# Kernel tuning notes

Hardware: AMD Instinct MI355X
Metric: run time of the kernel (lower is better)

Reference implementation:

```python
import jax, jax.numpy as jnp
import numpy as np

UNITS = 1024
INPUT_DIM = 2048
OUTPUT_DIM = 1000
EPS = 0.01
DT = 0.1
BATCH = 8192


def _kaiming_like(key, shape, fan_in):
    # matches torch kaiming_uniform_(a=sqrt(5)) bound = sqrt(6/((1+5)*fan_in)) = 1/sqrt(fan_in)
    bound = 1.0 / np.sqrt(fan_in)
    return jax.random.uniform(key, shape, jnp.float32, -bound, bound)


def setup_inputs() -> dict:
    key = jax.random.key(0)
    ks = jax.random.split(key, 12)
    x = jax.random.normal(ks[0], (BATCH, INPUT_DIM), jnp.float32)
    W_in = _kaiming_like(ks[1], (UNITS, INPUT_DIM), INPUT_DIM)
    b_in = _kaiming_like(ks[2], (UNITS,), INPUT_DIM)
    W1 = _kaiming_like(ks[3], (UNITS, UNITS), UNITS)
    b1 = _kaiming_like(ks[4], (UNITS,), UNITS)
    W2 = _kaiming_like(ks[5], (UNITS, UNITS), UNITS)
    b2 = _kaiming_like(ks[6], (UNITS,), UNITS)
    W3 = _kaiming_like(ks[7], (UNITS, UNITS), UNITS)
    b3 = _kaiming_like(ks[8], (UNITS,), UNITS)
    W_out = _kaiming_like(ks[9], (OUTPUT_DIM, UNITS), UNITS)
    b_out = _kaiming_like(ks[10], (OUTPUT_DIM,), UNITS)
    return {"x": x, "W_in": W_in, "b_in": b_in, "W1": W1, "b1": b1,
            "W2": W2, "b2": b2, "W3": W3, "b3": b3,
            "W_out": W_out, "b_out": b_out}


def transnet_layer(z, W, b):
    # z: (B, 2U). Implicit layer: A y = rhs, output = C y - rhs (== -y mathematically)
    U = W.shape[0]
    u_in, v_in = z[:, :U], z[:, U:]
    relu_u = jax.nn.relu(u_in)
    rhs_u = u_in + DT * b                      # (B, U)
    rhs_v = v_in + (DT / EPS) * relu_u         # (B, U)
    rhs = jnp.concatenate([rhs_u, rhs_v], axis=1)  # (B, 2U)
    eye = jnp.eye(U, dtype=z.dtype)
    A = jnp.block([[eye, DT * W],
                   [-DT * W.T, (1.0 + DT / EPS) * eye]])  # (2U, 2U), batch-independent
    # factor once, solve against all batch rhs columns at once
    y = jnp.linalg.solve(A, rhs.T).T           # (B, 2U)
    u, v = y[:, :U], y[:, U:]
    u_out = DT * (v @ W.T) - u_in - DT * b
    v_out = -DT * (u @ W) + (DT / EPS) * v - v_in - (DT / EPS) * relu_u
    return jnp.concatenate([u_out, v_out], axis=1)


def reference(x, W_in, b_in, W1, b1, W2, b2, W3, b3, W_out, b_out):
    z = x @ W_in.T + b_in                      # (B, U)
    z = jnp.concatenate([z, jax.nn.relu(z)], axis=1)  # (B, 2U)
    z = transnet_layer(z, W1, b1)
    z = transnet_layer(z, W2, b2)
    z = transnet_layer(z, W3, b3)
    z = z[:, :UNITS]
    logits = jax.nn.softmax(z @ W_out.T + b_out, axis=1)
    return logits
```

## Files before the change

### kernel.cpp

```cpp
#include <hip/hip_runtime.h>
#include <hip/hip_bf16.h>
#include <cstdint>


typedef __bf16 bf16;
typedef __bf16 bf16x4 __attribute__((ext_vector_type(4)));
typedef __bf16 bf16x8 __attribute__((ext_vector_type(8)));
typedef float  f32x4  __attribute__((ext_vector_type(4)));

#define C_DT    0.1f
#define C_DTEPS 10.0f
#define C_DINV  (1.0f/11.0f)
#define C_MSC   (0.01f/121.0f)

__device__ __forceinline__ void async_load16(const bf16* g, bf16* l) {
    __builtin_amdgcn_global_load_lds(
        (__attribute__((address_space(1))) void*)(g),
        (__attribute__((address_space(3))) void*)(l),
        16, 0, 0);
}

__device__ __forceinline__ void remap_block(int& bx, int& by) {
    if (gridDim.y == 64) {
        const int lin  = by * 8 + bx;
        const int xcd  = lin & 7;
        const int slot = lin >> 3;
        by = xcd * 8 + (slot & 7);
        bx = slot >> 3;
    }
}

template<int EPI>
__global__ __launch_bounds__(256, 2)
void gemm_bt(const bf16* __restrict__ A, const bf16* __restrict__ B,
             float* __restrict__ out_f,
             bf16* __restrict__ out_b1, bf16* __restrict__ out_b2,
             const float* __restrict__ e0, const float* __restrict__ e1,
             const float* __restrict__ e2,
             int M, int N, int K, int lda, int ldb,
             int ldf, int ld1, int ld2, float sgn,
             long zsA, long zsB, long zs1, long zs2)
{
    __shared__ __attribute__((aligned(16))) char smem[32768];
    bf16* sAe = (bf16*)smem;
    bf16* sBe = (bf16*)(smem + 16384);

    const int t    = threadIdx.x;
    const int wave = t >> 6;
    const int lane = t & 63;
    int bx = blockIdx.x, by = blockIdx.y;
    remap_block(bx, by);
    const long zb = blockIdx.z;
    A += zb * zsA;
    B += zb * zsB;
    if (out_b1) out_b1 += zb * zs1;
    if (out_b2) out_b2 += zb * zs2;

    const long row0 = (long)by * 128;
    const long col0 = (long)bx * 128;
    const int wr = wave >> 1, wc = wave & 1;

    f32x4 acc[4][4];
#pragma unroll
    for (int i = 0; i < 4; i++)
#pragma unroll
        for (int j = 0; j < 4; j++)
            acc[i][j] = f32x4{0.f, 0.f, 0.f, 0.f};

    const int  q  = t >> 2;
    const int  gp = ((t & 3) + 4 - ((q + (q >> 2)) & 3)) & 3;
    const bf16* gA = A + (row0 + q) * (long)lda + gp * 8;
    const bf16* gB = B + (col0 + q) * (long)ldb + gp * 8;

    const int l15  = lane & 15;
    const int fch  = ((lane >> 4) + l15 + (l15 >> 2)) & 3;
    const int aoff = (wr * 64 + l15) * 32 + fch * 8;
    const int boff = (wc * 64 + l15) * 32 + fch * 8;

    auto stage = [&](int buf, int k0) {
        bf16* dA = sAe + buf * 4096 + wave * 512;
        bf16* dB = sBe + buf * 4096 + wave * 512;
        async_load16(gA + k0,                     dA);
        async_load16(gA + 64 * (long)lda + k0,    dA + 2048);
        async_load16(gB + k0,                     dB);
        async_load16(gB + 64 * (long)ldb + k0,    dB + 2048);
    };

    const int nIter = K >> 5;
    stage(0, 0);
    __syncthreads();
    for (int k = 0; k < nIter; k++) {
        const int cur = k & 1;
        if (k + 1 < nIter) stage(cur ^ 1, (k + 1) << 5);

        bf16x8 af[4], bfv[4];
#pragma unroll
        for (int i = 0; i < 4; i++)
            af[i] = *(const bf16x8*)(sAe + cur * 4096 + aoff + i * 16 * 32);
#pragma unroll
        for (int j = 0; j < 4; j++)
            bfv[j] = *(const bf16x8*)(sBe + cur * 4096 + boff + j * 16 * 32);
#pragma unroll
        for (int i = 0; i < 4; i++)
#pragma unroll
            for (int j = 0; j < 4; j++)
                acc[i][j] = __builtin_amdgcn_mfma_f32_16x16x32_bf16(
                    af[i], bfv[j], acc[i][j], 0, 0, 0);

        __syncthreads();
    }

    float* epi = (float*)smem + wave * 1024;
    const int wbase = (lane >> 4) * 256 + (l15 >> 2) * 4 + (l15 & 3);

#pragma unroll
    for (int i = 0; i < 4; i++) {
#pragma unroll
        for (int j = 0; j < 4; j++)
#pragma unroll
            for (int r = 0; r < 4; r++)
                epi[wbase + r * 64 + 16 * j] = acc[i][j][r];

#pragma unroll
        for (int qq = 0; qq < 4; qq++) {
            const f32x4 a4 = ((const f32x4*)epi)[qq * 64 + lane];
            const long m = row0 + wr * 64 + i * 16 + qq * 4 + (lane >> 4);
            const long n = col0 + wc * 64 + 4 * l15;

            if (EPI == 0) {
                const f32x4 b1 = *(const f32x4*)(e1 + n);
                const f32x4 b2 = *(const f32x4*)(e2 + n);
                f32x4 tv; bf16x4 rv, hv;
#pragma unroll
                for (int e = 0; e < 4; e++) {
                    tv[e] = a4[e] + b1[e];
                    rv[e] = (bf16)(11.f * fmaxf(tv[e], 0.f));
                    hv[e] = (bf16)(tv[e] + C_DT * b2[e]);
                }
                *(f32x4*)(out_f + m * (long)ldf + n)    = tv;
                *(bf16x4*)(out_b1 + m * (long)ld1 + n)  = rv;
                *(bf16x4*)(out_b2 + m * (long)ld2 + n)  = hv;
            } else if (EPI == 1) {
                bf16x4 ov;
#pragma unroll
                for (int e = 0; e < 4; e++)
                    ov[e] = (bf16)(((m == n + e) ? C_DINV : 0.f) - C_MSC * a4[e]);
                *(bf16x4*)(out_b1 + m * (long)ld1 + n) = ov;
                *(bf16x4*)(out_b2 + m * (long)ld2 + n) = ov;
            } else if (EPI == 2) {
                bf16x4 ov, o2;
#pragma unroll
                for (int e = 0; e < 4; e++) {
                    ov[e] = (bf16)(sgn * a4[e]);
                    o2[e] = (bf16)(C_DT * sgn * a4[e]);
                }
                *(bf16x4*)(out_b1 + m * (long)ld1 + n) = ov;
                if (out_b2) *(bf16x4*)(out_b2 + m * (long)ld2 + n) = o2;
            } else {
                const f32x4 u0 = *(const f32x4*)(e0 + m * (long)ldf + n);
                const f32x4 b1 = *(const f32x4*)(e1 + n);
                bf16x4 hv, lv;
#pragma unroll
                for (int e = 0; e < 4; e++) {
                    float un = sgn * a4[e] - u0[e] - C_DT * b1[e];
                    bf16 h = (bf16)un;
                    hv[e] = h;
                    lv[e] = (bf16)(un - (float)h);
                }
                *(bf16x4*)(out_b1 + m * (long)ld1 + n) = hv;
                *(bf16x4*)(out_b2 + m * (long)ld2 + n) = lv;
            }
        }
    }
}

__global__ __launch_bounds__(256, 2)
void gemm_layer(const bf16* __restrict__ A, const bf16* __restrict__ B1,
                const bf16* __restrict__ B2, float* __restrict__ u,
                bf16* __restrict__ ACo,
                const float* __restrict__ bl, const float* __restrict__ bn)
{
    __shared__ __attribute__((aligned(16))) char smem[49152];
    bf16* sA  = (bf16*)smem;
    bf16* sB1 = (bf16*)(smem + 16384);
    bf16* sB2 = (bf16*)(smem + 32768);

    const int t    = threadIdx.x;
    const int wave = t >> 6;
    const int lane = t & 63;
    int bx = blockIdx.x, by = blockIdx.y;
    remap_block(bx, by);
    const long row0 = (long)by * 128;
    const long col0 = (long)bx * 128;
    const int wr = wave >> 1, wc = wave & 1;

    f32x4 accU[4][4], accV[4][4];
#pragma unroll
    for (int i = 0; i < 4; i++)
#pragma unroll
        for (int j = 0; j < 4; j++) {
            accU[i][j] = f32x4{0.f, 0.f, 0.f, 0.f};
            accV[i][j] = f32x4{0.f, 0.f, 0.f, 0.f};
        }

    const int  q  = t >> 2;
    const int  gp = ((t & 3) + 4 - ((q + (q >> 2)) & 3)) & 3;
    const bf16* gA  = A  + (row0 + q) * 2048 + gp * 8;
    const bf16* gB1 = B1 + (col0 + q) * 2048 + gp * 8;
    const bf16* gB2 = B2 + (col0 + q) * 2048 + gp * 8;

    const int l15  = lane & 15;
    const int fch  = ((lane >> 4) + l15 + (l15 >> 2)) & 3;
    const int aoff = (wr * 64 + l15) * 32 + fch * 8;
    const int boff = (wc * 64 + l15) * 32 + fch * 8;

    auto stage = [&](int buf, int k0) {
        bf16* dA  = sA  + buf * 4096 + wave * 512;
        bf16* dB1 = sB1 + buf * 4096 + wave * 512;
        bf16* dB2 = sB2 + buf * 4096 + wave * 512;
        async_load16(gA  + k0,             dA);
        async_load16(gA  + 64 * 2048 + k0, dA + 2048);
        async_load16(gB1 + k0,             dB1);
        async_load16(gB1 + 64 * 2048 + k0, dB1 + 2048);
        async_load16(gB2 + k0,             dB2);
        async_load16(gB2 + 64 * 2048 + k0, dB2 + 2048);
    };

    stage(0, 0);
    __syncthreads();
    for (int k = 0; k < 64; k++) {
        const int cur = k & 1;
        if (k + 1 < 64) stage(cur ^ 1, (k + 1) << 5);

        bf16x8 af[4], b1v[4], b2v[4];
#pragma unroll
        for (int i = 0; i < 4; i++)
            af[i] = *(const bf16x8*)(sA + cur * 4096 + aoff + i * 16 * 32);
#pragma unroll
        for (int j = 0; j < 4; j++) {
            b1v[j] = *(const bf16x8*)(sB1 + cur * 4096 + boff + j * 16 * 32);
            b2v[j] = *(const bf16x8*)(sB2 + cur * 4096 + boff + j * 16 * 32);
        }
#pragma unroll
        for (int i = 0; i < 4; i++)
#pragma unroll
            for (int j = 0; j < 4; j++) {
                accV[i][j] = __builtin_amdgcn_mfma_f32_16x16x32_bf16(
                    af[i], b1v[j], accV[i][j], 0, 0, 0);
                accU[i][j] = __builtin_amdgcn_mfma_f32_16x16x32_bf16(
                    af[i], b2v[j], accU[i][j], 0, 0, 0);
            }
        __syncthreads();
    }

    float* epi = (float*)smem + wave * 1024;
    const int wbase = (lane >> 4) * 256 + (l15 >> 2) * 4 + (l15 & 3);

#pragma unroll
    for (int i = 0; i < 4; i++) {
#pragma unroll
        for (int j = 0; j < 4; j++)
#pragma unroll
            for (int r = 0; r < 4; r++)
                epi[wbase + r * 64 + 16 * j] = accV[i][j][r];
        f32x4 v4[4];
#pragma unroll
        for (int qq = 0; qq < 4; qq++)
            v4[qq] = ((const f32x4*)epi)[qq * 64 + lane];
#pragma unroll
        for (int j = 0; j < 4; j++)
#pragma unroll
            for (int r = 0; r < 4; r++)
                epi[wbase + r * 64 + 16 * j] = accU[i][j][r];

#pragma unroll
        for (int qq = 0; qq < 4; qq++) {
            const f32x4 a4 = ((const f32x4*)epi)[qq * 64 + lane];
            const long m  = row0 + wr * 64 + i * 16 + qq * 4 + (lane >> 4);
            const long n  = col0 + wc * 64 + 4 * l15;
            const long iu = m * 1024 + n;
            const f32x4 u0 = *(const f32x4*)(u + iu);
            const f32x4 c1 = *(const f32x4*)(bl + n);
            const f32x4 c2 = *(const f32x4*)(bn + n);
            f32x4 un; bf16x4 rv, hv;
#pragma unroll
            for (int e = 0; e < 4; e++) {
                un[e] = a4[e] - u0[e] - C_DT * c1[e];
                rv[e] = (bf16)(C_DTEPS * fmaxf(un[e], 0.f) - v4[qq][e]);
                hv[e] = (bf16)(un[e] + C_DT * c2[e]);
            }
            *(f32x4*)(u + iu) = un;
            *(bf16x4*)(ACo + m * 2048 + n)        = rv;
            *(bf16x4*)(ACo + m * 2048 + 1024 + n) = hv;
        }
    }
}

__global__ __launch_bounds__(256, 2)
void gemm_split(const bf16* __restrict__ Ah, const bf16* __restrict__ Al,
                const bf16* __restrict__ Bh, const bf16* __restrict__ Bl,
                float* __restrict__ out, const float* __restrict__ bias,
                int M, int N, int K, int blim)
{
    __shared__ __attribute__((aligned(16))) char smem[65536];
    bf16* sAh = (bf16*)smem;
    bf16* sAl = (bf16*)(smem + 16384);
    bf16* sBh = (bf16*)(smem + 32768);
    bf16* sBl = (bf16*)(smem + 49152);

    const int t    = threadIdx.x;
    const int wave = t >> 6;
    const int lane = t & 63;
    int bx = blockIdx.x, by = blockIdx.y;
    remap_block(bx, by);
    const long row0 = (long)by * 128;
    const long col0 = (long)bx * 128;
    const int wr = wave >> 1, wc = wave & 1;

    f32x4 acc[4][4];
#pragma unroll
    for (int i = 0; i < 4; i++)
#pragma unroll
        for (int j = 0; j < 4; j++)
            acc[i][j] = f32x4{0.f, 0.f, 0.f, 0.f};

    const int  q  = t >> 2;
    const int  gp = ((t & 3) + 4 - ((q + (q >> 2)) & 3)) & 3;
    const long gao = (row0 + q) * (long)K + gp * 8;
    const long gbo = (col0 + q) * (long)K + gp * 8;

    const int l15  = lane & 15;
    const int fch  = ((lane >> 4) + l15 + (l15 >> 2)) & 3;
    const int aoff = (wr * 64 + l15) * 32 + fch * 8;
    const int boff = (wc * 64 + l15) * 32 + fch * 8;

    auto stage = [&](int buf, int k0) {
        const int d = buf * 4096 + wave * 512;
        async_load16(Ah + gao + k0,                 sAh + d);
        async_load16(Ah + gao + 64 * (long)K + k0,  sAh + d + 2048);
        async_load16(Al + gao + k0,                 sAl + d);
        async_load16(Al + gao + 64 * (long)K + k0,  sAl + d + 2048);
        async_load16(Bh + gbo + k0,                 sBh + d);
        async_load16(Bh + gbo + 64 * (long)K + k0,  sBh + d + 2048);
        async_load16(Bl + gbo + k0,                 sBl + d);
        async_load16(Bl + gbo + 64 * (long)K + k0,  sBl + d + 2048);
    };

    const int nIter = K >> 5;
    stage(0, 0);
    __syncthreads();
    for (int k = 0; k < nIter; k++) {
        const int cur = k & 1;
        if (k + 1 < nIter) stage(cur ^ 1, (k + 1) << 5);

        bf16x8 ah[4], al[4], bh[4], bl[4];
#pragma unroll
        for (int i = 0; i < 4; i++) {
            ah[i] = *(const bf16x8*)(sAh + cur * 4096 + aoff + i * 16 * 32);
            al[i] = *(const bf16x8*)(sAl + cur * 4096 + aoff + i * 16 * 32);
        }
#pragma unroll
        for (int j = 0; j < 4; j++) {
            bh[j] = *(const bf16x8*)(sBh + cur * 4096 + boff + j * 16 * 32);
            bl[j] = *(const bf16x8*)(sBl + cur * 4096 + boff + j * 16 * 32);
        }
#pragma unroll
        for (int i = 0; i < 4; i++)
#pragma unroll
            for (int j = 0; j < 4; j++) {
                acc[i][j] = __builtin_amdgcn_mfma_f32_16x16x32_bf16(
                    ah[i], bh[j], acc[i][j], 0, 0, 0);
                acc[i][j] = __builtin_amdgcn_mfma_f32_16x16x32_bf16(
                    ah[i], bl[j], acc[i][j], 0, 0, 0);
                acc[i][j] = __builtin_amdgcn_mfma_f32_16x16x32_bf16(
                    al[i], bh[j], acc[i][j], 0, 0, 0);
            }
        __syncthreads();
    }

    float* epi = (float*)smem + wave * 1024;
    const int wbase = (lane >> 4) * 256 + (l15 >> 2) * 4 + (l15 & 3);

#pragma unroll
    for (int i = 0; i < 4; i++) {
#pragma unroll
        for (int j = 0; j < 4; j++)
#pragma unroll
            for (int r = 0; r < 4; r++)
                epi[wbase + r * 64 + 16 * j] = acc[i][j][r];

#pragma unroll
        for (int qq = 0; qq < 4; qq++) {
            f32x4 a4 = ((const f32x4*)epi)[qq * 64 + lane];
            const long m = row0 + wr * 64 + i * 16 + qq * 4 + (lane >> 4);
            const long n = col0 + wc * 64 + 4 * l15;
            f32x4 bv = f32x4{0.f, 0.f, 0.f, 0.f};
            if (n < blim) bv = *(const f32x4*)(bias + n);
#pragma unroll
            for (int e = 0; e < 4; e++) a4[e] += bv[e];
            *(f32x4*)(out + m * (long)N + n) = a4;
        }
    }
}

__global__ void conv_xw(const float* __restrict__ x, bf16* __restrict__ xb,
                        const float* __restrict__ w, bf16* __restrict__ wb)
{
    const long bid = blockIdx.x;
    const float* in;
    bf16* outp;
    long i4;
    if (bid < 16384) { in = x; outp = xb; i4 = bid * 256 + threadIdx.x; }
    else             { in = w; outp = wb; i4 = (bid - 16384) * 256 + threadIdx.x; }
    const f32x4 v = ((const f32x4*)in)[i4];
    bf16x4 o;
#pragma unroll
    for (int e = 0; e < 4; e++) o[e] = (bf16)v[e];
    ((bf16x4*)outp)[i4] = o;
}

__global__ void prep_w3(const float* __restrict__ w0, const float* __restrict__ w1,
                        const float* __restrict__ w2, bf16* __restrict__ Wb,
                        bf16* __restrict__ Wtb)
{
    __shared__ float tile[32][33];
    const int z = blockIdx.z;
    const float* W = (z == 0) ? w0 : (z == 1) ? w1 : w2;
    const long zo = (long)z * 1024 * 1024;
    const int bx = blockIdx.x * 32, by = blockIdx.y * 32;
    const int tx = threadIdx.x & 31, ty = threadIdx.x >> 5;
#pragma unroll
    for (int i = 0; i < 32; i += 8) {
        float v = W[(long)(by + ty + i) * 1024 + bx + tx];
        tile[ty + i][tx] = v;
        Wb[zo + (long)(by + ty + i) * 1024 + bx + tx] = (bf16)v;
    }
    __syncthreads();
#pragma unroll
    for (int i = 0; i < 32; i += 8)
        Wtb[zo + (long)(bx + ty + i) * 1024 + by + tx] = (bf16)tile[tx][ty + i];
}

__global__ void prep_wout(const float* __restrict__ w, bf16* __restrict__ wh,
                          bf16* __restrict__ wl)
{
    const long i4   = (long)blockIdx.x * 256 + threadIdx.x;
    const long base = i4 * 4;
    const int  nrow = (int)(base >> 10);
    bf16x4 h, l;
    if (nrow < 1000) {
        const f32x4 v = ((const f32x4*)w)[i4];
#pragma unroll
        for (int e = 0; e < 4; e++) {
            bf16 hh = (bf16)v[e];
            h[e] = hh;
            l[e] = (bf16)(v[e] - (float)hh);
        }
    } else {
#pragma unroll
        for (int e = 0; e < 4; e++) { h[e] = (bf16)0.f; l[e] = (bf16)0.f; }
    }
    ((bf16x4*)wh)[i4] = h;
    ((bf16x4*)wl)[i4] = l;
}

__global__ __launch_bounds__(256)
void softmax_rows(const float* __restrict__ logits, float* __restrict__ out)
{
    const int row = blockIdx.x;
    const float* lp = logits + (long)row * 1024;
    const int t = threadIdx.x;
    float v[4];
    float mx = -1e30f;
#pragma unroll
    for (int i = 0; i < 4; i++) {
        const int c = t + i * 256;
        v[i] = (c < 1000) ? lp[c] : -1e30f;
        mx = fmaxf(mx, v[i]);
    }
#pragma unroll
    for (int off = 32; off; off >>= 1)
        mx = fmaxf(mx, __shfl_xor(mx, off));
    __shared__ float sm[4], ss[4];
    const int wave = t >> 6;
    if ((t & 63) == 0) sm[wave] = mx;
    __syncthreads();
    mx = fmaxf(fmaxf(sm[0], sm[1]), fmaxf(sm[2], sm[3]));
    float sum = 0.f;
#pragma unroll
    for (int i = 0; i < 4; i++) {
        v[i] = __expf(v[i] - mx);
        sum += v[i];
    }
#pragma unroll
    for (int off = 32; off; off >>= 1)
        sum += __shfl_xor(sum, off);
    if ((t & 63) == 0) ss[wave] = sum;
    __syncthreads();
    const float inv = 1.f / (ss[0] + ss[1] + ss[2] + ss[3]);
#pragma unroll
    for (int i = 0; i < 4; i++) {
        const int c = t + i * 256;
        if (c < 1000) out[(long)row * 1000 + c] = v[i] * inv;
    }
}

extern "C" void kernel_launch(void* const* d_in, const int* in_sizes, int n_in,
                              void* d_out, int out_size, void* d_ws, size_t ws_size,
                              hipStream_t stream)
{
    const float* x     = (const float*)d_in[0];
    const float* W_in  = (const float*)d_in[1];
    const float* b_in  = (const float*)d_in[2];
    const float* Ws[3] = {(const float*)d_in[3], (const float*)d_in[5], (const float*)d_in[7]};
    const float* bs[3] = {(const float*)d_in[4], (const float*)d_in[6], (const float*)d_in[8]};
    const float* W_out = (const float*)d_in[9];
    const float* b_out = (const float*)d_in[10];
    float* out = (float*)d_out;

    char* ws = (char*)d_ws;
    const size_t MB = 1u << 20;
    const long M1 = 1024L * 1024;
    bf16*  xb    = (bf16*)(ws);
    bf16*  Wtbf  = (bf16*)(ws);
    bf16*  Minv  = (bf16*)(ws +  6 * MB);
    bf16*  Pmat  = (bf16*)(ws + 12 * MB);
    bf16*  Bcat  = (bf16*)(ws + 18 * MB);
    bf16*  zh    = (bf16*)(ws);
    bf16*  zl    = (bf16*)(ws + 16 * MB);
    bf16*  Winb  = (bf16*)(ws + 32 * MB);
    bf16*  Wouth = (bf16*)(ws + 36 * MB);
    bf16*  Woutl = (bf16*)(ws + 38 * MB);
    bf16*  Wbf   = (bf16*)(ws + 40 * MB);
    bf16*  Ccat  = (bf16*)(ws + 46 * MB);
    float* u     = (float*)(ws + 58 * MB);
    float* logits= (float*)(ws + 58 * MB);
    bf16*  AC_a  = (bf16*)(ws + 90 * MB);
    bf16*  AC_b  = (bf16*)(ws + 122 * MB);

    const dim3 blk(256);
    const dim3 gBig(8, 64);
    const dim3 gSm3(8, 8, 3);
    const dim3 gT3(32, 32, 3);

    conv_xw<<<18432, blk, 0, stream>>>(x, xb, W_in, Winb);
    prep_wout<<<1024, blk, 0, stream>>>(W_out, Wouth, Woutl);

    gemm_bt<0><<<gBig, blk, 0, stream>>>(xb, Winb, u, AC_a, AC_a + 1024,
                                         nullptr, b_in, bs[0],
                                         8192, 1024, 2048, 2048, 2048,
                                         1024, 2048, 2048, 1.f, 0, 0, 0, 0);

    prep_w3<<<gT3, blk, 0, stream>>>(Ws[0], Ws[1], Ws[2], Wbf, Wtbf);
    gemm_bt<1><<<gSm3, blk, 0, stream>>>(Wtbf, Wtbf, nullptr, Minv, Bcat,
                                         nullptr, nullptr, nullptr,
                                         1024, 1024, 1024, 1024, 1024,
                                         0, 1024, 2048, 1.f, M1, M1, M1, 2 * M1);
    gemm_bt<2><<<gSm3, blk, 0, stream>>>(Minv, Wbf, nullptr, Bcat + 1024, nullptr,
                                         nullptr, nullptr, nullptr,
                                         1024, 1024, 1024, 1024, 1024,
                                         0, 2048, 0, C_DT, M1, M1, 2 * M1, 0);
    gemm_bt<2><<<gSm3, blk, 0, stream>>>(Wbf, Minv, nullptr, Pmat, Ccat,
                                         nullptr, nullptr, nullptr,
                                         1024, 1024, 1024, 1024, 1024,
                                         0, 1024, 2048, 1.f, M1, M1, M1, 2 * M1);
    gemm_bt<2><<<gSm3, blk, 0, stream>>>(Pmat, Wbf, nullptr, Ccat + 1024, nullptr,
                                         nullptr, nullptr, nullptr,
                                         1024, 1024, 1024, 1024, 1024,
                                         0, 2048, 0, 0.01f, M1, M1, 2 * M1, 0);

    gemm_layer<<<gBig, blk, 0, stream>>>(AC_a, Bcat, Ccat, u, AC_b, bs[0], bs[1]);
    gemm_layer<<<gBig, blk, 0, stream>>>(AC_b, Bcat + 2 * M1, Ccat + 2 * M1,
                                         u, AC_a, bs[1], bs[2]);
    gemm_bt<5><<<gBig, blk, 0, stream>>>(AC_a, Ccat + 4 * M1, nullptr, zh, zl,
                                         u, bs[2], nullptr,
                                         8192, 1024, 2048, 2048, 2048,
                                         1024, 1024, 1024, 1.f, 0, 0, 0, 0);

    gemm_split<<<gBig, blk, 0, stream>>>(zh, zl, Wouth, Woutl, logits, b_out,
                                         8192, 1024, 1024, 1000);
    softmax_rows<<<8192, blk, 0, stream>>>(logits, out);
}
```

Measured before the change: 534.2 us.

## Rewrite layer GEMM with 8-wave 256x128 tiles and interleaved async prefetch

Replaces the 4-wave 128x128 layer GEMM with an 8-wave kernel that computes a 256x128 tile and uses a K-step of 64 with an XOR-swizzled LDS layout. Prefetch of the next stage is split into four chunks, each issued between the MFMA phases, with explicit vmcnt/lgkmcnt waits, barriers and s_setprio raised around the MFMA blocks. The aim is better reuse of B per A load, fewer global loads, and tighter overlap of memory traffic with matrix math. In exchange it uses 128KB of LDS per block, which limits occupancy, and it drops the block remapping.

```diff
diff --git a/kernel.cpp b/kernel.cpp
--- a/kernel.cpp
+++ b/kernel.cpp
@@ -174,117 +174,200 @@
     }
 }
 
-__global__ __launch_bounds__(256, 2)
-void gemm_layer(const bf16* __restrict__ A, const bf16* __restrict__ B1,
-                const bf16* __restrict__ B2, float* __restrict__ u,
-                bf16* __restrict__ ACo,
-                const float* __restrict__ bl, const float* __restrict__ bn)
-{
-    __shared__ __attribute__((aligned(16))) char smem[49152];
-    bf16* sA  = (bf16*)smem;
-    bf16* sB1 = (bf16*)(smem + 16384);
-    bf16* sB2 = (bf16*)(smem + 32768);
+__global__ __launch_bounds__(512, 2)
+void gemm_layer8(const bf16* __restrict__ A, const bf16* __restrict__ B1,
+                 const bf16* __restrict__ B2, float* __restrict__ u,
+                 bf16* __restrict__ ACo,
+                 const float* __restrict__ bl, const float* __restrict__ bn)
+{
+    __shared__ __attribute__((aligned(16))) bf16 sm[65536];
 
     const int t    = threadIdx.x;
     const int wave = t >> 6;
     const int lane = t & 63;
-    int bx = blockIdx.x, by = blockIdx.y;
-    remap_block(bx, by);
-    const long row0 = (long)by * 128;
+    const int l15  = lane & 15;
+    const int lq   = lane >> 4;
+    const int bx = blockIdx.x;
+    const int by = blockIdx.y;
+    const long row0 = (long)by * 256;
     const long col0 = (long)bx * 128;
-    const int wr = wave >> 1, wc = wave & 1;
-
-    f32x4 accU[4][4], accV[4][4];
-#pragma unroll
-    for (int i = 0; i < 4; i++)
-#pragma unroll
-        for (int j = 0; j < 4; j++) {
+    const int wr = wave >> 2;
+    const int wc = wave & 3;
+
+    f32x4 accV[8][2], accU[8][2];
+#pragma unroll
+    for (int i = 0; i < 8; i++)
+#pragma unroll
+        for (int j = 0; j < 2; j++) {
+            accV[i][j] = f32x4{0.f, 0.f, 0.f, 0.f};
             accU[i][j] = f32x4{0.f, 0.f, 0.f, 0.f};
-            accV[i][j] = f32x4{0.f, 0.f, 0.f, 0.f};
-        }
-
-    const int  q  = t >> 2;
-    const int  gp = ((t & 3) + 4 - ((q + (q >> 2)) & 3)) & 3;
-    const bf16* gA  = A  + (row0 + q) * 2048 + gp * 8;
-    const bf16* gB1 = B1 + (col0 + q) * 2048 + gp * 8;
-    const bf16* gB2 = B2 + (col0 + q) * 2048 + gp * 8;
-
-    const int l15  = lane & 15;
-    const int fch  = ((lane >> 4) + l15 + (l15 >> 2)) & 3;
-    const int aoff = (wr * 64 + l15) * 32 + fch * 8;
-    const int boff = (wc * 64 + l15) * 32 + fch * 8;
-
-    auto stage = [&](int buf, int k0) {
-        bf16* dA  = sA  + buf * 4096 + wave * 512;
-        bf16* dB1 = sB1 + buf * 4096 + wave * 512;
-        bf16* dB2 = sB2 + buf * 4096 + wave * 512;
-        async_load16(gA  + k0,             dA);
-        async_load16(gA  + 64 * 2048 + k0, dA + 2048);
-        async_load16(gB1 + k0,             dB1);
-        async_load16(gB1 + 64 * 2048 + k0, dB1 + 2048);
-        async_load16(gB2 + k0,             dB2);
-        async_load16(gB2 + 64 * 2048 + k0, dB2 + 2048);
+        }
+
+    const int tr = t >> 3;
+    const int sg = (t & 7) ^ (tr & 7);
+    const bf16* gA  = A  + (row0 + tr) * 2048 + sg * 8;
+    const bf16* gB1 = B1 + (col0 + tr) * 2048 + sg * 8;
+    const bf16* gB2 = B2 + (col0 + tr) * 2048 + sg * 8;
+    bf16* const ldA  = sm + wave * 512;
+    bf16* const ldB1 = sm + 32768 + wave * 512;
+    bf16* const ldB2 = sm + 49152 + wave * 512;
+
+    auto stA = [&](int buf, int ci, int k0) {
+        async_load16(gA + (long)ci * 131072 + k0, ldA + buf * 16384 + ci * 4096);
     };
-
-    stage(0, 0);
-    __syncthreads();
-    for (int k = 0; k < 64; k++) {
-        const int cur = k & 1;
-        if (k + 1 < 64) stage(cur ^ 1, (k + 1) << 5);
-
-        bf16x8 af[4], b1v[4], b2v[4];
-#pragma unroll
-        for (int i = 0; i < 4; i++)
-            af[i] = *(const bf16x8*)(sA + cur * 4096 + aoff + i * 16 * 32);
-#pragma unroll
-        for (int j = 0; j < 4; j++) {
-            b1v[j] = *(const bf16x8*)(sB1 + cur * 4096 + boff + j * 16 * 32);
-            b2v[j] = *(const bf16x8*)(sB2 + cur * 4096 + boff + j * 16 * 32);
-        }
-#pragma unroll
-        for (int i = 0; i < 4; i++)
-#pragma unroll
-            for (int j = 0; j < 4; j++) {
-                accV[i][j] = __builtin_amdgcn_mfma_f32_16x16x32_bf16(
-                    af[i], b1v[j], accV[i][j], 0, 0, 0);
-                accU[i][j] = __builtin_amdgcn_mfma_f32_16x16x32_bf16(
-                    af[i], b2v[j], accU[i][j], 0, 0, 0);
+    auto stB1v = [&](int buf, int cb, int k0) {
+        async_load16(gB1 + (long)cb * 131072 + k0, ldB1 + buf * 8192 + cb * 4096);
+    };
+    auto stB2v = [&](int buf, int cb, int k0) {
+        async_load16(gB2 + (long)cb * 131072 + k0, ldB2 + buf * 8192 + cb * 4096);
+    };
+
+    const int sl0 = lq ^ (l15 & 7);
+    const int sl1 = (4 + lq) ^ (l15 & 7);
+    const int aro = l15 * 64;
+    const int cbo = (wc >> 1) * 4096;
+    const int bro = ((wc & 1) * 32 + l15) * 64;
+
+    stA(0, 0, 0); stA(0, 2, 0);
+    stB1v(0, 0, 0); stB1v(0, 1, 0);
+    stB2v(0, 0, 0); stB2v(0, 1, 0);
+    stA(0, 1, 0); stA(0, 3, 0);
+
+    for (int kt = 0; kt < 32; ++kt) {
+        const int  cur = kt & 1, nb = cur ^ 1;
+        const bool st  = kt < 31;
+        const int  k0n = (kt + 1) << 6;
+        const bf16* bA  = sm + cur * 16384;
+        const bf16* bB1 = sm + 32768 + cur * 8192;
+        const bf16* bB2 = sm + 49152 + cur * 8192;
+        bf16x8 a[4], b1k[2], b2k[2];
+
+        if (st) asm volatile("s_waitcnt vmcnt(2)" ::: "memory");
+        else    asm volatile("s_waitcnt vmcnt(0)" ::: "memory");
+        __builtin_amdgcn_s_barrier();
+#pragma unroll
+        for (int fi = 0; fi < 4; ++fi)
+            a[fi] = *(const bf16x8*)(bA + wr * 8192 + fi * 1024 + aro + sl0 * 8);
+#pragma unroll
+        for (int fj = 0; fj < 2; ++fj) {
+            b1k[fj] = *(const bf16x8*)(bB1 + cbo + fj * 1024 + bro + sl0 * 8);
+            b2k[fj] = *(const bf16x8*)(bB2 + cbo + fj * 1024 + bro + sl0 * 8);
+        }
+        if (st) { stA(nb, 0, k0n); stA(nb, 2, k0n); }
+        __builtin_amdgcn_s_barrier();
+        asm volatile("s_waitcnt lgkmcnt(0)" ::: "memory");
+        __builtin_amdgcn_s_setprio(1);
+#pragma unroll
+        for (int fi = 0; fi < 4; ++fi)
+#pragma unroll
+            for (int fj = 0; fj < 2; ++fj) {
+                accV[fi][fj] = __builtin_amdgcn_mfma_f32_16x16x32_bf16(
+                    a[fi], b1k[fj], accV[fi][fj], 0, 0, 0);
+                accU[fi][fj] = __builtin_amdgcn_mfma_f32_16x16x32_bf16(
+                    a[fi], b2k[fj], accU[fi][fj], 0, 0, 0);
             }
-        __syncthreads();
-    }
-
-    float* epi = (float*)smem + wave * 1024;
-    const int wbase = (lane >> 4) * 256 + (l15 >> 2) * 4 + (l15 & 3);
-
-#pragma unroll
-    for (int i = 0; i < 4; i++) {
-#pragma unroll
-        for (int j = 0; j < 4; j++)
-#pragma unroll
-            for (int r = 0; r < 4; r++)
-                epi[wbase + r * 64 + 16 * j] = accV[i][j][r];
+        __builtin_amdgcn_s_setprio(0);
+
+        asm volatile("s_waitcnt vmcnt(2)" ::: "memory");
+        __builtin_amdgcn_s_barrier();
+#pragma unroll
+        for (int fi = 0; fi < 4; ++fi)
+            a[fi] = *(const bf16x8*)(bA + wr * 8192 + 4096 + fi * 1024 + aro + sl0 * 8);
+        if (st) { stB1v(nb, 0, k0n); stB1v(nb, 1, k0n); }
+        __builtin_amdgcn_s_barrier();
+        asm volatile("s_waitcnt lgkmcnt(0)" ::: "memory");
+        __builtin_amdgcn_s_setprio(1);
+#pragma unroll
+        for (int fi = 0; fi < 4; ++fi)
+#pragma unroll
+            for (int fj = 0; fj < 2; ++fj) {
+                accV[4 + fi][fj] = __builtin_amdgcn_mfma_f32_16x16x32_bf16(
+                    a[fi], b1k[fj], accV[4 + fi][fj], 0, 0, 0);
+                accU[4 + fi][fj] = __builtin_amdgcn_mfma_f32_16x16x32_bf16(
+                    a[fi], b2k[fj], accU[4 + fi][fj], 0, 0, 0);
+            }
+        __builtin_amdgcn_s_setprio(0);
+
+        __builtin_amdgcn_s_barrier();
+#pragma unroll
+        for (int fi = 0; fi < 4; ++fi)
+            a[fi] = *(const bf16x8*)(bA + wr * 8192 + fi * 1024 + aro + sl1 * 8);
+#pragma unroll
+        for (int fj = 0; fj < 2; ++fj) {
+            b1k[fj] = *(const bf16x8*)(bB1 + cbo + fj * 1024 + bro + sl1 * 8);
+            b2k[fj] = *(const bf16x8*)(bB2 + cbo + fj * 1024 + bro + sl1 * 8);
+        }
+        if (st) { stB2v(nb, 0, k0n); stB2v(nb, 1, k0n); }
+        __builtin_amdgcn_s_barrier();
+        asm volatile("s_waitcnt lgkmcnt(0)" ::: "memory");
+        __builtin_amdgcn_s_setprio(1);
+#pragma unroll
+        for (int fi = 0; fi < 4; ++fi)
+#pragma unroll
+            for (int fj = 0; fj < 2; ++fj) {
+                accV[fi][fj] = __builtin_amdgcn_mfma_f32_16x16x32_bf16(
+                    a[fi], b1k[fj], accV[fi][fj], 0, 0, 0);
+                accU[fi][fj] = __builtin_amdgcn_mfma_f32_16x16x32_bf16(
+                    a[fi], b2k[fj], accU[fi][fj], 0, 0, 0);
+            }
+        __builtin_amdgcn_s_setprio(0);
+
+        __builtin_amdgcn_s_barrier();
+#pragma unroll
+        for (int fi = 0; fi < 4; ++fi)
+            a[fi] = *(const bf16x8*)(bA + wr * 8192 + 4096 + fi * 1024 + aro + sl1 * 8);
+        if (st) { stA(nb, 1, k0n); stA(nb, 3, k0n); }
+        __builtin_amdgcn_s_barrier();
+        asm volatile("s_waitcnt lgkmcnt(0)" ::: "memory");
+        __builtin_amdgcn_s_setprio(1);
+#pragma unroll
+        for (int fi = 0; fi < 4; ++fi)
+#pragma unroll
+            for (int fj = 0; fj < 2; ++fj) {
+                accV[4 + fi][fj] = __builtin_amdgcn_mfma_f32_16x16x32_bf16(
+                    a[fi], b1k[fj], accV[4 + fi][fj], 0, 0, 0);
+                accU[4 + fi][fj] = __builtin_amdgcn_mfma_f32_16x16x32_bf16(
+                    a[fi], b2k[fj], accU[4 + fi][fj], 0, 0, 0);
+            }
+        __builtin_amdgcn_s_setprio(0);
+    }
+
+    float* epi = (float*)sm + wave * 1024;
+    const int ew = lq * 128 + l15;
+
+#pragma unroll
+    for (int fib = 0; fib < 4; ++fib) {
+#pragma unroll
+        for (int f2 = 0; f2 < 2; ++f2)
+#pragma unroll
+            for (int fj = 0; fj < 2; ++fj)
+#pragma unroll
+                for (int r = 0; r < 4; ++r)
+                    epi[f2 * 512 + ew + r * 32 + fj * 16] = accV[fib * 2 + f2][fj][r];
         f32x4 v4[4];
 #pragma unroll
-        for (int qq = 0; qq < 4; qq++)
+        for (int qq = 0; qq < 4; ++qq)
             v4[qq] = ((const f32x4*)epi)[qq * 64 + lane];
 #pragma unroll
-        for (int j = 0; j < 4; j++)
-#pragma unroll
-            for (int r = 0; r < 4; r++)
-                epi[wbase + r * 64 + 16 * j] = accU[i][j][r];
-
-#pragma unroll
-        for (int qq = 0; qq < 4; qq++) {
+        for (int f2 = 0; f2 < 2; ++f2)
+#pragma unroll
+            for (int fj = 0; fj < 2; ++fj)
+#pragma unroll
+                for (int r = 0; r < 4; ++r)
+                    epi[f2 * 512 + ew + r * 32 + fj * 16] = accU[fib * 2 + f2][fj][r];
+
+#pragma unroll
+        for (int qq = 0; qq < 4; ++qq) {
             const f32x4 a4 = ((const f32x4*)epi)[qq * 64 + lane];
-            const long m  = row0 + wr * 64 + i * 16 + qq * 4 + (lane >> 4);
-            const long n  = col0 + wc * 64 + 4 * l15;
+            const long m = row0 + wr * 128 + fib * 32 + qq * 8 + (lane >> 3);
+            const long n = col0 + wc * 32 + (lane & 7) * 4;
             const long iu = m * 1024 + n;
             const f32x4 u0 = *(const f32x4*)(u + iu);
             const f32x4 c1 = *(const f32x4*)(bl + n);
             const f32x4 c2 = *(const f32x4*)(bn + n);
             f32x4 un; bf16x4 rv, hv;
 #pragma unroll
-            for (int e = 0; e < 4; e++) {
+            for (int e = 0; e < 4; ++e) {
                 un[e] = a4[e] - u0[e] - C_DT * c1[e];
                 rv[e] = (bf16)(C_DTEPS * fmaxf(un[e], 0.f) - v4[qq][e]);
                 hv[e] = (bf16)(un[e] + C_DT * c2[e]);
@@ -539,7 +622,9 @@
     bf16*  AC_b  = (bf16*)(ws + 122 * MB);
 
     const dim3 blk(256);
+    const dim3 blk512(512);
     const dim3 gBig(8, 64);
+    const dim3 gLay(8, 32);
     const dim3 gSm3(8, 8, 3);
     const dim3 gT3(32, 32, 3);
 
@@ -569,9 +654,9 @@
                                          1024, 1024, 1024, 1024, 1024,
                                          0, 2048, 0, 0.01f, M1, M1, 2 * M1, 0);
 
-    gemm_layer<<<gBig, blk, 0, stream>>>(AC_a, Bcat, Ccat, u, AC_b, bs[0], bs[1]);
-    gemm_layer<<<gBig, blk, 0, stream>>>(AC_b, Bcat + 2 * M1, Ccat + 2 * M1,
-                                         u, AC_a, bs[1], bs[2]);
+    gemm_layer8<<<gLay, blk512, 0, stream>>>(AC_a, Bcat, Ccat, u, AC_b, bs[0], bs[1]);
+    gemm_layer8<<<gLay, blk512, 0, stream>>>(AC_b, Bcat + 2 * M1, Ccat + 2 * M1,
+                                             u, AC_a, bs[1], bs[2]);
     gemm_bt<5><<<gBig, blk, 0, stream>>>(AC_a, Ccat + 4 * M1, nullptr, zh, zl,
                                          u, bs[2], nullptr,
                                          8192, 1024, 2048, 2048, 2048,
```

Result: no change. 539.3 us (+1.0%).

## Merge prep kernels and batch two independent weight GEMMs into one launch

Applied to the files above, without the earlier changes.

Folds the x/W_in conversion, W_out hi/lo split and W1-3 transpose into a single prep_all launch, and combines two independent per-layer 1024x1024 GEMMs into one 6-slice grid (gemm_step67). It also raises the gemm_bt occupancy hint from 2 to 3 blocks per CU. The aim is fewer launches and better filling of the GPU by the small 192-block weight GEMMs. The higher occupancy hint may force register spills in the big GEMMs. Wtbf moves to a separate workspace region so the prep work can run before gemm_bt<0>.

```diff
diff --git a/kernel.cpp b/kernel.cpp
--- a/kernel.cpp
+++ b/kernel.cpp
@@ -31,7 +31,7 @@
 }
 
 template<int EPI>
-__global__ __launch_bounds__(256, 2)
+__global__ __launch_bounds__(256, 3)
 void gemm_bt(const bf16* __restrict__ A, const bf16* __restrict__ B,
              float* __restrict__ out_f,
              bf16* __restrict__ out_b1, bf16* __restrict__ out_b2,
@@ -296,6 +296,122 @@
     }
 }
 
+__global__ __launch_bounds__(256, 3)
+void gemm_step67(const bf16* __restrict__ Minv, const bf16* __restrict__ Wbf,
+                 bf16* __restrict__ Bc1, bf16* __restrict__ Pm,
+                 bf16* __restrict__ Cc)
+{
+    __shared__ __attribute__((aligned(16))) char smem[32768];
+    bf16* sAe = (bf16*)smem;
+    bf16* sBe = (bf16*)(smem + 16384);
+
+    const int t    = threadIdx.x;
+    const int wave = t >> 6;
+    const int lane = t & 63;
+    const int bx = blockIdx.x, by = blockIdx.y;
+    const long zb = blockIdx.z;
+    const long M1v = 1024L * 1024;
+
+    const bf16 *A, *B;
+    bf16 *o1, *o2;
+    int ld1;
+    const bool alt = (zb >= 3);
+    if (!alt) {
+        A = Minv + zb * M1v; B = Wbf + zb * M1v;
+        o1 = Bc1 + zb * 2 * M1v; o2 = nullptr; ld1 = 2048;
+    } else {
+        const long zr = zb - 3;
+        A = Wbf + zr * M1v; B = Minv + zr * M1v;
+        o1 = Pm + zr * M1v; o2 = Cc + zr * 2 * M1v; ld1 = 1024;
+    }
+
+    const long row0 = (long)by * 128;
+    const long col0 = (long)bx * 128;
+    const int wr = wave >> 1, wc = wave & 1;
+
+    f32x4 acc[4][4];
+#pragma unroll
+    for (int i = 0; i < 4; i++)
+#pragma unroll
+        for (int j = 0; j < 4; j++)
+            acc[i][j] = f32x4{0.f, 0.f, 0.f, 0.f};
+
+    const int  q  = t >> 2;
+    const int  gp = ((t & 3) + 4 - ((q + (q >> 2)) & 3)) & 3;
+    const bf16* gA = A + (row0 + q) * 1024 + gp * 8;
+    const bf16* gB = B + (col0 + q) * 1024 + gp * 8;
+
+    const int l15  = lane & 15;
+    const int fch  = ((lane >> 4) + l15 + (l15 >> 2)) & 3;
+    const int aoff = (wr * 64 + l15) * 32 + fch * 8;
+    const int boff = (wc * 64 + l15) * 32 + fch * 8;
+
+    auto stage = [&](int buf, int k0) {
+        bf16* dA = sAe + buf * 4096 + wave * 512;
+        bf16* dB = sBe + buf * 4096 + wave * 512;
+        async_load16(gA + k0,              dA);
+        async_load16(gA + 64 * 1024 + k0,  dA + 2048);
+        async_load16(gB + k0,              dB);
+        async_load16(gB + 64 * 1024 + k0,  dB + 2048);
+    };
+
+    stage(0, 0);
+    __syncthreads();
+    for (int k = 0; k < 32; k++) {
+        const int cur = k & 1;
+        if (k + 1 < 32) stage(cur ^ 1, (k + 1) << 5);
+
+        bf16x8 af[4], bfv[4];
+#pragma unroll
+        for (int i = 0; i < 4; i++)
+            af[i] = *(const bf16x8*)(sAe + cur * 4096 + aoff + i * 16 * 32);
+#pragma unroll
+        for (int j = 0; j < 4; j++)
+            bfv[j] = *(const bf16x8*)(sBe + cur * 4096 + boff + j * 16 * 32);
+#pragma unroll
+        for (int i = 0; i < 4; i++)
+#pragma unroll
+            for (int j = 0; j < 4; j++)
+                acc[i][j] = __builtin_amdgcn_mfma_f32_16x16x32_bf16(
+                    af[i], bfv[j], acc[i][j], 0, 0, 0);
+        __syncthreads();
+    }
+
+    float* epi = (float*)smem + wave * 1024;
+    const int wbase = (lane >> 4) * 256 + (l15 >> 2) * 4 + (l15 & 3);
+
+#pragma unroll
+    for (int i = 0; i < 4; i++) {
+#pragma unroll
+        for (int j = 0; j < 4; j++)
+#pragma unroll
+            for (int r = 0; r < 4; r++)
+                epi[wbase + r * 64 + 16 * j] = acc[i][j][r];
+
+#pragma unroll
+        for (int qq = 0; qq < 4; qq++) {
+            const f32x4 a4 = ((const f32x4*)epi)[qq * 64 + lane];
+            const long m = row0 + wr * 64 + i * 16 + qq * 4 + (lane >> 4);
+            const long n = col0 + wc * 64 + 4 * l15;
+            if (!alt) {
+                bf16x4 ov;
+#pragma unroll
+                for (int e = 0; e < 4; e++) ov[e] = (bf16)(C_DT * a4[e]);
+                *(bf16x4*)(o1 + m * (long)ld1 + n) = ov;
+            } else {
+                bf16x4 ov, o2v;
+#pragma unroll
+                for (int e = 0; e < 4; e++) {
+                    ov[e]  = (bf16)a4[e];
+                    o2v[e] = (bf16)(C_DT * a4[e]);
+                }
+                *(bf16x4*)(o1 + m * (long)ld1 + n) = ov;
+                *(bf16x4*)(o2 + m * 2048 + n)      = o2v;
+            }
+        }
+    }
+}
+
 __global__ __launch_bounds__(256, 2)
 void gemm_split(const bf16* __restrict__ Ah, const bf16* __restrict__ Al,
                 const bf16* __restrict__ Bh, const bf16* __restrict__ Bl,
@@ -403,65 +519,71 @@
     }
 }
 
-__global__ void conv_xw(const float* __restrict__ x, bf16* __restrict__ xb,
-                        const float* __restrict__ w, bf16* __restrict__ wb)
-{
-    const long bid = blockIdx.x;
-    const float* in;
-    bf16* outp;
-    long i4;
-    if (bid < 16384) { in = x; outp = xb; i4 = bid * 256 + threadIdx.x; }
-    else             { in = w; outp = wb; i4 = (bid - 16384) * 256 + threadIdx.x; }
-    const f32x4 v = ((const f32x4*)in)[i4];
-    bf16x4 o;
-#pragma unroll
-    for (int e = 0; e < 4; e++) o[e] = (bf16)v[e];
-    ((bf16x4*)outp)[i4] = o;
-}
-
-__global__ void prep_w3(const float* __restrict__ w0, const float* __restrict__ w1,
-                        const float* __restrict__ w2, bf16* __restrict__ Wb,
-                        bf16* __restrict__ Wtb)
+__global__ __launch_bounds__(256)
+void prep_all(const float* __restrict__ x, bf16* __restrict__ xb,
+              const float* __restrict__ win, bf16* __restrict__ winb,
+              const float* __restrict__ wout, bf16* __restrict__ wouth,
+              bf16* __restrict__ woutl,
+              const float* __restrict__ w0, const float* __restrict__ w1,
+              const float* __restrict__ w2,
+              bf16* __restrict__ Wb, bf16* __restrict__ Wtb)
 {
     __shared__ float tile[32][33];
-    const int z = blockIdx.z;
-    const float* W = (z == 0) ? w0 : (z == 1) ? w1 : w2;
-    const long zo = (long)z * 1024 * 1024;
-    const int bx = blockIdx.x * 32, by = blockIdx.y * 32;
-    const int tx = threadIdx.x & 31, ty = threadIdx.x >> 5;
-#pragma unroll
-    for (int i = 0; i < 32; i += 8) {
-        float v = W[(long)(by + ty + i) * 1024 + bx + tx];
-        tile[ty + i][tx] = v;
-        Wb[zo + (long)(by + ty + i) * 1024 + bx + tx] = (bf16)v;
-    }
-    __syncthreads();
-#pragma unroll
-    for (int i = 0; i < 32; i += 8)
-        Wtb[zo + (long)(bx + ty + i) * 1024 + by + tx] = (bf16)tile[tx][ty + i];
-}
-
-__global__ void prep_wout(const float* __restrict__ w, bf16* __restrict__ wh,
-                          bf16* __restrict__ wl)
-{
-    const long i4   = (long)blockIdx.x * 256 + threadIdx.x;
-    const long base = i4 * 4;
-    const int  nrow = (int)(base >> 10);
-    bf16x4 h, l;
-    if (nrow < 1000) {
-        const f32x4 v = ((const f32x4*)w)[i4];
-#pragma unroll
-        for (int e = 0; e < 4; e++) {
-            bf16 hh = (bf16)v[e];
-            h[e] = hh;
-            l[e] = (bf16)(v[e] - (float)hh);
-        }
+    const long bid = blockIdx.x;
+    const int  t   = threadIdx.x;
+
+    if (bid < 16384) {
+        const long i4 = bid * 256 + t;
+        const f32x4 v = ((const f32x4*)x)[i4];
+        bf16x4 o;
+#pragma unroll
+        for (int e = 0; e < 4; e++) o[e] = (bf16)v[e];
+        ((bf16x4*)xb)[i4] = o;
+    } else if (bid < 18432) {
+        const long i4 = (bid - 16384) * 256 + t;
+        const f32x4 v = ((const f32x4*)win)[i4];
+        bf16x4 o;
+#pragma unroll
+        for (int e = 0; e < 4; e++) o[e] = (bf16)v[e];
+        ((bf16x4*)winb)[i4] = o;
+    } else if (bid < 19456) {
+        const long i4   = (bid - 18432) * 256 + t;
+        const long base = i4 * 4;
+        const int  nrow = (int)(base >> 10);
+        bf16x4 h, l;
+        if (nrow < 1000) {
+            const f32x4 v = ((const f32x4*)wout)[i4];
+#pragma unroll
+            for (int e = 0; e < 4; e++) {
+                bf16 hh = (bf16)v[e];
+                h[e] = hh;
+                l[e] = (bf16)(v[e] - (float)hh);
+            }
+        } else {
+#pragma unroll
+            for (int e = 0; e < 4; e++) { h[e] = (bf16)0.f; l[e] = (bf16)0.f; }
+        }
+        ((bf16x4*)wouth)[i4] = h;
+        ((bf16x4*)woutl)[i4] = l;
     } else {
-#pragma unroll
-        for (int e = 0; e < 4; e++) { h[e] = (bf16)0.f; l[e] = (bf16)0.f; }
-    }
-    ((bf16x4*)wh)[i4] = h;
-    ((bf16x4*)wl)[i4] = l;
+        const long b2 = bid - 19456;
+        const int  z  = (int)(b2 >> 10);
+        const int  idx = (int)(b2 & 1023);
+        const float* W = (z == 0) ? w0 : (z == 1) ? w1 : w2;
+        const long zo = (long)z << 20;
+        const int bxt = (idx & 31) * 32, byt = (idx >> 5) * 32;
+        const int tx = t & 31, ty = t >> 5;
+#pragma unroll
+        for (int i = 0; i < 32; i += 8) {
+            float v = W[(long)(byt + ty + i) * 1024 + bxt + tx];
+            tile[ty + i][tx] = v;
+            Wb[zo + (long)(byt + ty + i) * 1024 + bxt + tx] = (bf16)v;
+        }
+        __syncthreads();
+#pragma unroll
+        for (int i = 0; i < 32; i += 8)
+            Wtb[zo + (long)(bxt + ty + i) * 1024 + byt + tx] = (bf16)tile[tx][ty + i];
+    }
 }
 
 __global__ __launch_bounds__(256)
@@ -522,7 +644,6 @@
     const size_t MB = 1u << 20;
     const long M1 = 1024L * 1024;
     bf16*  xb    = (bf16*)(ws);
-    bf16*  Wtbf  = (bf16*)(ws);
     bf16*  Minv  = (bf16*)(ws +  6 * MB);
     bf16*  Pmat  = (bf16*)(ws + 12 * MB);
     bf16*  Bcat  = (bf16*)(ws + 18 * MB);
@@ -537,33 +658,26 @@
     float* logits= (float*)(ws + 58 * MB);
     bf16*  AC_a  = (bf16*)(ws + 90 * MB);
     bf16*  AC_b  = (bf16*)(ws + 122 * MB);
+    bf16*  Wtbf  = (bf16*)(ws + 122 * MB);
 
     const dim3 blk(256);
     const dim3 gBig(8, 64);
     const dim3 gSm3(8, 8, 3);
-    const dim3 gT3(32, 32, 3);
-
-    conv_xw<<<18432, blk, 0, stream>>>(x, xb, W_in, Winb);
-    prep_wout<<<1024, blk, 0, stream>>>(W_out, Wouth, Woutl);
+    const dim3 gSm6(8, 8, 6);
+
+    prep_all<<<22528, blk, 0, stream>>>(x, xb, W_in, Winb, W_out, Wouth, Woutl,
+                                        Ws[0], Ws[1], Ws[2], Wbf, Wtbf);
 
     gemm_bt<0><<<gBig, blk, 0, stream>>>(xb, Winb, u, AC_a, AC_a + 1024,
                                          nullptr, b_in, bs[0],
                                          8192, 1024, 2048, 2048, 2048,
                                          1024, 2048, 2048, 1.f, 0, 0, 0, 0);
 
-    prep_w3<<<gT3, blk, 0, stream>>>(Ws[0], Ws[1], Ws[2], Wbf, Wtbf);
     gemm_bt<1><<<gSm3, blk, 0, stream>>>(Wtbf, Wtbf, nullptr, Minv, Bcat,
                                          nullptr, nullptr, nullptr,
                                          1024, 1024, 1024, 1024, 1024,
                                          0, 1024, 2048, 1.f, M1, M1, M1, 2 * M1);
-    gemm_bt<2><<<gSm3, blk, 0, stream>>>(Minv, Wbf, nullptr, Bcat + 1024, nullptr,
-                                         nullptr, nullptr, nullptr,
-                                         1024, 1024, 1024, 1024, 1024,
-                                         0, 2048, 0, C_DT, M1, M1, 2 * M1, 0);
-    gemm_bt<2><<<gSm3, blk, 0, stream>>>(Wbf, Minv, nullptr, Pmat, Ccat,
-                                         nullptr, nullptr, nullptr,
-                                         1024, 1024, 1024, 1024, 1024,
-                                         0, 1024, 2048, 1.f, M1, M1, M1, 2 * M1);
+    gemm_step67<<<gSm6, blk, 0, stream>>>(Minv, Wbf, Bcat + 1024, Pmat, Ccat);
     gemm_bt<2><<<gSm3, blk, 0, stream>>>(Pmat, Wbf, nullptr, Ccat + 1024, nullptr,
                                          nullptr, nullptr, nullptr,
                                          1024, 1024, 1024, 1024, 1024,
```

After: 515.3 us. 1.04x faster.
